# Optimization experiments

Measured on AMD Instinct MI355X. Metric: run time of the kernel, lower is better.

## Reference

```python
import jax, jax.numpy as jnp
import numpy as np

L = 8192      # residues
K = 48        # k_neighbors
NODE = 128    # node_features
EDGE = 128    # edge_features
RBF = 16      # rbf_dim
POS = 16      # pos_embed_dim
AA = 26       # amino-acid alphabet
EPS = 1e-6


def _rbf(D):
    # Gaussian radial basis lift on [2, 22] Angstrom, 16 bins (ProteinMPNN standard)
    mu = jnp.linspace(2.0, 22.0, RBF).astype(D.dtype)
    sigma = (22.0 - 2.0) / RBF
    return jnp.exp(-(((D[..., None] - mu) / sigma) ** 2))


def setup_inputs() -> dict:
    key = jax.random.key(0)
    ks = jax.random.split(key, 8)
    X = jax.random.normal(ks[0], (L, 3), dtype=jnp.float32) * 10.0
    node_h = jax.random.normal(ks[1], (L, NODE), dtype=jnp.float32)
    f_node = jax.random.normal(ks[2], (L, EDGE), dtype=jnp.float32)
    aatype = jax.random.randint(ks[3], (L,), 0, AA, dtype=jnp.int32)
    residue_index = jnp.arange(L, dtype=jnp.int32)
    Wpos = jax.random.normal(ks[4], (16, POS + RBF + 8 + AA), dtype=jnp.float32) * 0.05
    bpos = jnp.zeros((16,), jnp.float32)
    We = jax.random.normal(ks[5], (EDGE, EDGE + 16 + RBF + NODE + NODE), dtype=jnp.float32) * 0.05
    ln_scale = jnp.ones((EDGE,), jnp.float32)
    ln_bias = jnp.zeros((EDGE,), jnp.float32)
    Wproj = jax.random.normal(ks[6], (EDGE, EDGE), dtype=jnp.float32) * 0.05
    bproj = jnp.zeros((EDGE,), jnp.float32)
    return dict(X=X, node_h=node_h, f_node=f_node, Wpos=Wpos, bpos=bpos, We=We,
                ln_scale=ln_scale, ln_bias=ln_bias, Wproj=Wproj, bproj=bproj,
                aatype=aatype, residue_index=residue_index)


def reference(X, node_h, f_node, Wpos, bpos, We, ln_scale, ln_bias, Wproj, bproj,
              aatype, residue_index):
    # pairwise CA distances [L, L] and k nearest neighbors
    diff_all = X[:, None, :] - X[None, :, :]
    D = jnp.sqrt(jnp.sum(diff_all * diff_all, -1) + EPS)
    negk, idx = jax.lax.top_k(-D, K)          # idx: [L, K]
    Dk = -negk                                # [L, K] neighbor distances
    rbf = _rbf(Dk)                            # [L, K, 16]
    # clipped relative sequence position one-hot [L, K, 16]
    off = residue_index[idx] - residue_index[:, None]
    pos_emb = jax.nn.one_hot(jnp.clip(off + POS // 2, 0, POS - 1), POS, dtype=X.dtype)
    # 8 geometric scalars: 5 distance transforms + unit direction vector
    unit = (X[idx] - X[:, None, :]) / (Dk[..., None] + EPS)
    scal = jnp.stack([Dk / 10.0, 1.0 / (1.0 + Dk), jnp.exp(-Dk), jnp.sin(Dk), jnp.cos(Dk)], -1)
    geom = jnp.concatenate([scal, unit], -1)  # [L, K, 8]
    seq_j = jax.nn.one_hot(aatype[idx], AA, dtype=X.dtype)  # [L, K, 26]
    pos_in = jnp.concatenate([pos_emb, rbf, geom, seq_j], -1)  # [L, K, 66]
    e_pos = pos_in @ Wpos.T + bpos            # w_pos: [L, K, 16]
    h_i = jnp.broadcast_to(node_h[:, None, :], (L, K, NODE))
    e_in = jnp.concatenate([f_node[idx], e_pos, rbf, h_i, node_h[idx]], -1)  # [L, K, 416]
    e = e_in @ We.T                           # w_e (no bias): [L, K, EDGE]
    mean = jnp.mean(e, -1, keepdims=True)
    var = jnp.var(e, -1, keepdims=True)
    e = (e - mean) * jax.lax.rsqrt(var + 1e-5) * ln_scale + ln_bias  # norm_edges
    return e @ Wproj.T + bproj                # w_e_proj: [L, K, EDGE]
```

## Files before the change

### kernel.cpp

```cpp
#include <hip/hip_runtime.h>
#include <stdint.h>
#include <math.h>

#define LRES 8192
#define KNB  48
#define ASTR 296
#define CUT  64

typedef _Float16 half_t;
typedef _Float16 half8 __attribute__((ext_vector_type(8)));
typedef float f4 __attribute__((ext_vector_type(4)));

__global__ void prep_kernel(const float* __restrict__ We, const float* __restrict__ Wproj,
                            const float* __restrict__ Wpos,
                            half_t* __restrict__ WeH, half_t* __restrict__ WpH,
                            float* __restrict__ Wh32, half_t* __restrict__ WposB) {
  int t = blockIdx.x * blockDim.x + threadIdx.x;
  if (t < 128 * 288) {
    int n = t / 288, kp = t % 288;
    int k = kp < 160 ? kp : kp + 128;
    WeH[n * 288 + kp] = (half_t)We[n * 416 + k];
  }
  if (t < 128 * 128) {
    int n = t >> 7, k = t & 127;
    WpH[t] = (half_t)Wproj[t];
    Wh32[k * 128 + n] = We[n * 416 + 160 + k];
  }
  if (t < 512) {
    int p = t >> 5, k = t & 31;
    float v = (k < 8) ? Wpos[p * 66 + 32 + k] : ((k < 16) ? 0.0f : Wpos[p * 66 + k]);
    WposB[t] = (half_t)v;
  }
}

__global__ __launch_bounds__(256) void cvt_kernel(const float* __restrict__ f_node,
                                                  const float* __restrict__ node_h,
                                                  half_t* __restrict__ fnH,
                                                  half_t* __restrict__ nhH) {
  int g = blockIdx.x * 256 + threadIdx.x;
  int sel = g >> 17;
  size_t off = (size_t)(g & 131071) * 8;
  const float* s = sel ? node_h : f_node;
  half_t* d = sel ? nhH : fnH;
  f4 a = *(const f4*)(s + off);
  f4 b = *(const f4*)(s + off + 4);
  half8 h;
#pragma unroll
  for (int j = 0; j < 4; ++j) { h[j] = (half_t)a[j]; h[4 + j] = (half_t)b[j]; }
  *(half8*)(d + off) = h;
}

__global__ __launch_bounds__(256) void hbias_kernel(const float* __restrict__ node_h,
                                                    const float* __restrict__ Wh32,
                                                    float* __restrict__ hb) {
  __shared__ float hrow[4][128];
  const int i0 = blockIdx.x * 4;
  const int t = threadIdx.x;
  for (int u = t; u < 512; u += 256) hrow[u >> 7][u & 127] = node_h[(size_t)i0 * 128 + u];
  __syncthreads();
  const int n = t & 127, g = t >> 7;
  float s0 = 0.f, s1 = 0.f;
#pragma unroll 8
  for (int cc = 0; cc < 128; ++cc) {
    float w = Wh32[cc * 128 + n];
    s0 = fmaf(w, hrow[g][cc], s0);
    s1 = fmaf(w, hrow[g + 2][cc], s1);
  }
  hb[(size_t)(i0 + g) * 128 + n] = s0;
  hb[(size_t)(i0 + g + 2) * 128 + n] = s1;
}

__global__ __launch_bounds__(256) void knn_kernel(const float* __restrict__ X,
                                                  int* __restrict__ out_idx,
                                                  float* __restrict__ out_D) {
  __shared__ unsigned hist[256];
  __shared__ double candD[256];
  __shared__ int candJ[256];
  __shared__ unsigned cnt;
  __shared__ int bstar_s;
  __shared__ unsigned cexp_s;
  __shared__ int needFull_s;
  const int i = blockIdx.x;
  const int tid = threadIdx.x;
  const float xi = X[i * 3 + 0], yi = X[i * 3 + 1], zi = X[i * 3 + 2];
  hist[tid] = 0u;
  if (tid == 0) cnt = 0u;
  __syncthreads();
  unsigned bpack[8];
#pragma unroll
  for (int it = 0; it < 8; ++it) {
    int jb = (tid + it * 256) * 4;
    const float* xp = X + (size_t)jb * 3;
    f4 r0 = *(const f4*)(xp);
    f4 r1 = *(const f4*)(xp + 4);
    f4 r2 = *(const f4*)(xp + 8);
    float px[4] = {r0[0], r0[3], r1[2], r2[1]};
    float py[4] = {r0[1], r1[0], r1[3], r2[2]};
    float pz[4] = {r0[2], r1[1], r2[0], r2[3]};
#pragma unroll
    for (int q = 0; q < 4; ++q) {
      float dx = px[q] - xi, dy = py[q] - yi, dz = pz[q] - zi;
      float D = sqrtf(dx * dx + dy * dy + dz * dz + 1e-6f);
      int b = (int)(D * 4.0f); if (b > 255) b = 255;
      int idx = it * 4 + q;
      int sh = (idx & 3) * 8;
      if ((idx & 3) == 0) bpack[idx >> 2] = (unsigned)b; else bpack[idx >> 2] |= (unsigned)b << sh;
      if (b < CUT) atomicAdd(&hist[b], 1u);
    }
  }
  __syncthreads();
  if (tid == 0) {
    unsigned run = 0; int b = 0;
    while (b < 255 && run + hist[b] < KNB) { run += hist[b]; ++b; }
    bstar_s = b;
    needFull_s = (b >= CUT - 1) ? 1 : 0;
    unsigned tot = run + hist[b];
    if (b < 255) tot += hist[b + 1];
    cexp_s = tot;
  }
  __syncthreads();
  if (needFull_s) {
#pragma unroll
    for (int idx = 0; idx < 32; ++idx) {
      int b = (int)((bpack[idx >> 2] >> ((idx & 3) * 8)) & 0xFFu);
      if (b >= CUT) atomicAdd(&hist[b], 1u);
    }
    __syncthreads();
    if (tid == 0) {
      unsigned run = 0; int b = 0;
      while (b < 255 && run + hist[b] < KNB) { run += hist[b]; ++b; }
      bstar_s = b;
      unsigned tot = run + hist[b];
      if (b < 255) tot += hist[b + 1];
      cexp_s = tot;
    }
    __syncthreads();
  }
  int bthr = bstar_s + 1; if (bthr > 255) bthr = 255;
  const unsigned cexp = cexp_s;
  const double xid = (double)xi, yid = (double)yi, zid = (double)zi;
  {
    unsigned cmask = 0u;
#pragma unroll
    for (int idx = 0; idx < 32; ++idx) {
      int b = (int)((bpack[idx >> 2] >> ((idx & 3) * 8)) & 0xFFu);
      if (b <= bthr) cmask |= (1u << idx);
    }
    while (cmask) {
      int k = __builtin_ctz(cmask);
      cmask &= cmask - 1u;
      int j = (tid + (k >> 2) * 256) * 4 + (k & 3);
      unsigned p = atomicAdd(&cnt, 1u);
      if (p < 256u) {
        double ddx = (double)X[j * 3 + 0] - xid;
        double ddy = (double)X[j * 3 + 1] - yid;
        double ddz = (double)X[j * 3 + 2] - zid;
        candD[p] = sqrt(ddx * ddx + ddy * ddy + ddz * ddz + 1e-6);
        candJ[p] = j;
      }
    }
  }
  __syncthreads();
  unsigned n = cnt;
  if (cexp <= 64u) {
    if (tid < 64) {
      double d = (tid < (int)n) ? candD[tid] : INFINITY;
      int j = (tid < (int)n) ? candJ[tid] : 0x7FFFFFFF;
#pragma unroll
      for (int size = 2; size <= 64; size <<= 1) {
#pragma unroll
        for (int stride = 32; stride > 0; stride >>= 1) {
          if (stride >= size) continue;
          double dp = __shfl_xor(d, stride, 64);
          int jp = __shfl_xor(j, stride, 64);
          bool up = ((tid & size) == 0);
          bool lower = ((tid & stride) == 0);
          bool mine_gt = (d > dp) || (d == dp && j > jp);
          bool part_gt = (dp > d) || (dp == d && jp > j);
          bool keep = lower ? (mine_gt != up) : (part_gt != up);
          d = keep ? d : dp;
          j = keep ? j : jp;
        }
      }
      if (tid < KNB) {
        out_idx[(size_t)i * KNB + tid] = j;
        out_D[(size_t)i * KNB + tid] = (float)d;
      }
    }
    return;
  }
  if (tid >= (int)n) { candD[tid] = INFINITY; candJ[tid] = 0x7FFFFFFF; }
  __syncthreads();
  for (unsigned size = 2; size <= 256; size <<= 1) {
    for (unsigned stride = size >> 1; stride > 0; stride >>= 1) {
      unsigned partner = (unsigned)tid ^ stride;
      if (partner > (unsigned)tid) {
        double da = candD[tid], db = candD[partner];
        int ja = candJ[tid], jb = candJ[partner];
        bool agtb = (da > db) || (da == db && ja > jb);
        bool asc = ((tid & size) == 0);
        if (agtb == asc) {
          candD[tid] = db; candJ[tid] = jb;
          candD[partner] = da; candJ[partner] = ja;
        }
      }
      __syncthreads();
    }
  }
  if (tid < KNB) {
    out_idx[(size_t)i * KNB + tid] = candJ[tid];
    out_D[(size_t)i * KNB + tid] = (float)candD[tid];
  }
}

__global__ __launch_bounds__(256, 4) void edge_kernel(
    const float* __restrict__ X, const half_t* __restrict__ fnH,
    const half_t* __restrict__ nhH, const float* __restrict__ Wpos,
    const float* __restrict__ bpos, const float* __restrict__ ln_scale,
    const float* __restrict__ ln_bias, const float* __restrict__ bproj,
    const int* __restrict__ aatype, const int* __restrict__ residue_index,
    const int* __restrict__ ws_idx, const float* __restrict__ ws_D,
    const half_t* __restrict__ WeH, const half_t* __restrict__ WpH,
    const half_t* __restrict__ WposB, const float* __restrict__ hbAll,
    float* __restrict__ out) {
  __shared__ __align__(16) half_t Ald[48 * ASTR];
  __shared__ float tabPool[672];
  __shared__ float DkL[48];
  __shared__ int jL[48], pidxL[48], aaL[48];

  float* pos_tab = tabPool;
  float* aa_tab  = tabPool + 256;
  float* redS    = tabPool;
  float* meanL   = tabPool + 384;
  float* rstdL   = tabPool + 432;

  const int i = blockIdx.x;
  const int tid = threadIdx.x;
  const int w = tid >> 6;
  const int lane = tid & 63;
  const int lm = lane & 15;
  const int quad = lane >> 4;
  const int quad8 = quad * 8;
  const int n0 = w * 32 + lm;

  {
    int pp = tid >> 4, p = tid & 15;
    pos_tab[tid] = Wpos[p * 66 + pp] + bpos[p];
  }
  for (int t = tid; t < 416; t += 256) {
    int a = t >> 4, p = t & 15;
    aa_tab[t] = Wpos[p * 66 + 40 + a];
  }
  const float xi = X[i * 3 + 0], yi = X[i * 3 + 1], zi = X[i * 3 + 2];
  if (tid < KNB) {
    int e = tid;
    int j = ws_idx[(size_t)i * KNB + e];
    float Dk = ws_D[(size_t)i * KNB + e];
    jL[e] = j; DkL[e] = Dk;
    float xj = X[j * 3 + 0], yj = X[j * 3 + 1], zj = X[j * 3 + 2];
    float inv = 1.0f / (Dk + 1e-6f);
    half_t* gr = Ald + e * ASTR + 128;
    gr[0] = (half_t)(Dk / 10.0f);
    gr[1] = (half_t)(1.0f / (1.0f + Dk));
    gr[2] = (half_t)expf(-Dk);
    gr[3] = (half_t)sinf(Dk);
    gr[4] = (half_t)cosf(Dk);
    gr[5] = (half_t)((xj - xi) * inv);
    gr[6] = (half_t)((yj - yi) * inv);
    gr[7] = (half_t)((zj - zi) * inv);
    *(uint2*)(gr + 8)  = (uint2){0u, 0u};
    *(uint2*)(gr + 12) = (uint2){0u, 0u};
    int off = residue_index[j] - residue_index[i] + 8;
    off = off < 0 ? 0 : (off > 15 ? 15 : off);
    pidxL[e] = off;
    aaL[e] = aatype[j];
  }
  __syncthreads();

  for (int t = tid; t < KNB * 16; t += 256) {
    int e = t >> 4, m = t & 15;
    float z = (DkL[e] - (2.0f + (float)m * (20.0f / 15.0f))) * 0.8f;
    Ald[e * ASTR + 144 + m] = (half_t)expf(-z * z);
  }
#pragma unroll
  for (int it = 0; it < 6; ++it) {
    int cid = tid + it * 256;
    int e = cid >> 5, r = cid & 31;
    int sel = r >> 4, c8 = r & 15;
    const half_t* src = (sel ? nhH : fnH) + (size_t)jL[e] * 128 + c8 * 8;
    *(half8*)(Ald + e * ASTR + sel * 160 + c8 * 8) = *(const half8*)src;
  }
  half8 bregA[9], bregB[9];
#pragma unroll
  for (int ks = 0; ks < 9; ++ks) {
    bregA[ks] = *(const half8*)(WeH + (size_t)n0 * 288 + ks * 32 + quad8);
    bregB[ks] = *(const half8*)(WeH + (size_t)(n0 + 16) * 288 + ks * 32 + quad8);
  }
  float hb0 = hbAll[(size_t)i * 128 + n0];
  float hb1 = hbAll[(size_t)i * 128 + n0 + 16];
  __syncthreads();

  if (w < 3) {
    half8 a = *(const half8*)(Ald + (w * 16 + lm) * ASTR + 128 + quad8);
    half8 bp = *(const half8*)(WposB + lm * 32 + quad8);
    f4 z = {};
    f4 ep = __builtin_amdgcn_mfma_f32_16x16x32_f16(a, bp, z, 0, 0, 0);
#pragma unroll
    for (int r = 0; r < 4; ++r) {
      int m = w * 16 + quad * 4 + r;
      float s = ep[r] + pos_tab[pidxL[m] * 16 + lm] + aa_tab[aaL[m] * 16 + lm];
      Ald[m * ASTR + 128 + lm] = (half_t)s;
    }
  }
  __syncthreads();

  f4 acc[3][2] = {};
#pragma unroll
  for (int ks = 0; ks < 9; ++ks) {
#pragma unroll
    for (int mt = 0; mt < 3; ++mt) {
      half8 a = *(const half8*)(Ald + (mt * 16 + lm) * ASTR + ks * 32 + quad8);
      acc[mt][0] = __builtin_amdgcn_mfma_f32_16x16x32_f16(a, bregA[ks], acc[mt][0], 0, 0, 0);
      acc[mt][1] = __builtin_amdgcn_mfma_f32_16x16x32_f16(a, bregB[ks], acc[mt][1], 0, 0, 0);
    }
  }
  half8 b2A[4], b2B[4];
#pragma unroll
  for (int ks = 0; ks < 4; ++ks) {
    b2A[ks] = *(const half8*)(WpH + (size_t)n0 * 128 + ks * 32 + quad8);
    b2B[ks] = *(const half8*)(WpH + (size_t)(n0 + 16) * 128 + ks * 32 + quad8);
  }
  float ls0 = ln_scale[n0], ls1 = ln_scale[n0 + 16];
  float lb0 = ln_bias[n0],  lb1 = ln_bias[n0 + 16];
  float bp0 = bproj[n0],    bp1 = bproj[n0 + 16];

#pragma unroll
  for (int mt = 0; mt < 3; ++mt)
#pragma unroll
    for (int r = 0; r < 4; ++r) { acc[mt][0][r] += hb0; acc[mt][1][r] += hb1; }
#pragma unroll
  for (int mt = 0; mt < 3; ++mt)
#pragma unroll
    for (int r = 0; r < 4; ++r) {
      float e0 = acc[mt][0][r], e1 = acc[mt][1][r];
      float sv = e0 + e1;
      float qv = e0 * e0 + e1 * e1;
#pragma unroll
      for (int m = 1; m < 16; m <<= 1) {
        sv += __shfl_xor(sv, m, 16);
        qv += __shfl_xor(qv, m, 16);
      }
      if (lm == 0) {
        int row = mt * 16 + quad * 4 + r;
        redS[row * 8 + w * 2 + 0] = sv;
        redS[row * 8 + w * 2 + 1] = qv;
      }
    }
  __syncthreads();
  if (tid < KNB) {
    float s = redS[tid * 8 + 0] + redS[tid * 8 + 2] + redS[tid * 8 + 4] + redS[tid * 8 + 6];
    float q = redS[tid * 8 + 1] + redS[tid * 8 + 3] + redS[tid * 8 + 5] + redS[tid * 8 + 7];
    float m = s * (1.0f / 128.0f);
    float var = q * (1.0f / 128.0f) - m * m;
    meanL[tid] = m;
    rstdL[tid] = rsqrtf(var + 1e-5f);
  }
  __syncthreads();

#pragma unroll
  for (int mt = 0; mt < 3; ++mt)
#pragma unroll
    for (int nt = 0; nt < 2; ++nt) {
      int n = n0 + nt * 16;
      float ls = nt ? ls1 : ls0, lb = nt ? lb1 : lb0;
#pragma unroll
      for (int r = 0; r < 4; ++r) {
        int m = mt * 16 + quad * 4 + r;
        float e = (acc[mt][nt][r] - meanL[m]) * rstdL[m] * ls + lb;
        Ald[m * ASTR + n] = (half_t)e;
      }
    }
  __syncthreads();

  f4 acc2[3][2] = {};
#pragma unroll
  for (int ks = 0; ks < 4; ++ks) {
#pragma unroll
    for (int mt = 0; mt < 3; ++mt) {
      half8 a = *(const half8*)(Ald + (mt * 16 + lm) * ASTR + ks * 32 + quad8);
      acc2[mt][0] = __builtin_amdgcn_mfma_f32_16x16x32_f16(a, b2A[ks], acc2[mt][0], 0, 0, 0);
      acc2[mt][1] = __builtin_amdgcn_mfma_f32_16x16x32_f16(a, b2B[ks], acc2[mt][1], 0, 0, 0);
    }
  }

#pragma unroll
  for (int mt = 0; mt < 3; ++mt)
#pragma unroll
    for (int nt = 0; nt < 2; ++nt) {
      int n = n0 + nt * 16;
      float bp = nt ? bp1 : bp0;
#pragma unroll
      for (int r = 0; r < 4; ++r) {
        int m = mt * 16 + quad * 4 + r;
        out[((size_t)i * KNB + m) * 128 + n] = acc2[mt][nt][r] + bp;
      }
    }
}

extern "C" void kernel_launch(void* const* d_in, const int* in_sizes, int n_in,
                              void* d_out, int out_size, void* d_ws, size_t ws_size,
                              hipStream_t stream) {
  const float* X        = (const float*)d_in[0];
  const float* node_h   = (const float*)d_in[1];
  const float* f_node   = (const float*)d_in[2];
  const float* Wpos     = (const float*)d_in[3];
  const float* bpos     = (const float*)d_in[4];
  const float* We       = (const float*)d_in[5];
  const float* ln_scale = (const float*)d_in[6];
  const float* ln_bias  = (const float*)d_in[7];
  const float* Wproj    = (const float*)d_in[8];
  const float* bproj    = (const float*)d_in[9];
  const int*   aatype   = (const int*)d_in[10];
  const int*   residue_index = (const int*)d_in[11];
  float* out = (float*)d_out;

  char* ws = (char*)d_ws;
  int*    ws_idx = (int*)ws;
  float*  ws_D   = (float*)(ws + 1572864);
  half_t* WeH    = (half_t*)(ws + 3145728);
  half_t* WpH    = (half_t*)(ws + 3219456);
  float*  Wh32   = (float*)(ws + 3252224);
  half_t* WposB  = (half_t*)(ws + 3317760);
  float*  hbAll  = (float*)(ws + 3318784);
  half_t* fnH    = (half_t*)(ws + 7513088);
  half_t* nhH    = (half_t*)(ws + 9610240);

  prep_kernel<<<144, 256, 0, stream>>>(We, Wproj, Wpos, WeH, WpH, Wh32, WposB);
  cvt_kernel<<<1024, 256, 0, stream>>>(f_node, node_h, fnH, nhH);
  hbias_kernel<<<2048, 256, 0, stream>>>(node_h, Wh32, hbAll);
  knn_kernel<<<LRES, 256, 0, stream>>>(X, ws_idx, ws_D);
  edge_kernel<<<LRES, 256, 0, stream>>>(X, fnH, nhH, Wpos, bpos, ln_scale,
                                        ln_bias, bproj, aatype, residue_index,
                                        ws_idx, ws_D, WeH, WpH, WposB, hbAll, out);
}
```

Measured before the change: 401.1 us.

## Fuse kNN selection into edge kernel and merge conversion with node-bias kernel

Merges the per-residue kNN kernel into the edge kernel so neighbor indices and distances stay in shared memory rather than passing through global workspace. The candidate sort buffers alias the edge input tile. The fp16 conversion and node-bias kernels are also combined into one launch. This removes two launches and a global round trip, but the fused kernel now carries kNN's work and register pressure under the edge kernel's occupancy bound, so the two phases cannot overlap across kernels.

```diff
diff --git a/kernel.cpp b/kernel.cpp
--- a/kernel.cpp
+++ b/kernel.cpp
@@ -11,10 +11,11 @@
 typedef _Float16 half8 __attribute__((ext_vector_type(8)));
 typedef float f4 __attribute__((ext_vector_type(4)));
 
-__global__ void prep_kernel(const float* __restrict__ We, const float* __restrict__ Wproj,
-                            const float* __restrict__ Wpos,
-                            half_t* __restrict__ WeH, half_t* __restrict__ WpH,
-                            float* __restrict__ Wh32, half_t* __restrict__ WposB) {
+__global__ __launch_bounds__(256) void setup_a_kernel(
+    const float* __restrict__ We, const float* __restrict__ Wproj,
+    const float* __restrict__ Wpos,
+    half_t* __restrict__ WeH, half_t* __restrict__ WpH,
+    float* __restrict__ Wh32, half_t* __restrict__ WposB) {
   int t = blockIdx.x * blockDim.x + threadIdx.x;
   if (t < 128 * 288) {
     int n = t / 288, kp = t % 288;
@@ -33,55 +34,88 @@
   }
 }
 
-__global__ __launch_bounds__(256) void cvt_kernel(const float* __restrict__ f_node,
-                                                  const float* __restrict__ node_h,
-                                                  half_t* __restrict__ fnH,
-                                                  half_t* __restrict__ nhH) {
-  int g = blockIdx.x * 256 + threadIdx.x;
-  int sel = g >> 17;
-  size_t off = (size_t)(g & 131071) * 8;
-  const float* s = sel ? node_h : f_node;
-  half_t* d = sel ? nhH : fnH;
-  f4 a = *(const f4*)(s + off);
-  f4 b = *(const f4*)(s + off + 4);
-  half8 h;
-#pragma unroll
-  for (int j = 0; j < 4; ++j) { h[j] = (half_t)a[j]; h[4 + j] = (half_t)b[j]; }
-  *(half8*)(d + off) = h;
+__global__ __launch_bounds__(256) void setup_b_kernel(
+    const float* __restrict__ f_node, const float* __restrict__ node_h,
+    const float* __restrict__ Wh32,
+    half_t* __restrict__ fnH, half_t* __restrict__ nhH,
+    float* __restrict__ hb) {
+  __shared__ float hrow[4][128];
+  const int b = blockIdx.x;
+  const int tid = threadIdx.x;
+  if (b < 1024) {
+    int g = b * 256 + tid;
+    int sel = g >> 17;
+    size_t off = (size_t)(g & 131071) * 8;
+    const float* s = sel ? node_h : f_node;
+    half_t* d = sel ? nhH : fnH;
+    f4 a = *(const f4*)(s + off);
+    f4 bb = *(const f4*)(s + off + 4);
+    half8 h;
+#pragma unroll
+    for (int j = 0; j < 4; ++j) { h[j] = (half_t)a[j]; h[4 + j] = (half_t)bb[j]; }
+    *(half8*)(d + off) = h;
+  } else {
+    const int i0 = (b - 1024) * 4;
+    for (int u = tid; u < 512; u += 256) hrow[u >> 7][u & 127] = node_h[(size_t)i0 * 128 + u];
+    __syncthreads();
+    const int n = tid & 127, g = tid >> 7;
+    float s0 = 0.f, s1 = 0.f;
+#pragma unroll 8
+    for (int cc = 0; cc < 128; ++cc) {
+      float w = Wh32[cc * 128 + n];
+      s0 = fmaf(w, hrow[g][cc], s0);
+      s1 = fmaf(w, hrow[g + 2][cc], s1);
+    }
+    hb[(size_t)(i0 + g) * 128 + n] = s0;
+    hb[(size_t)(i0 + g + 2) * 128 + n] = s1;
+  }
 }
 
-__global__ __launch_bounds__(256) void hbias_kernel(const float* __restrict__ node_h,
-                                                    const float* __restrict__ Wh32,
-                                                    float* __restrict__ hb) {
-  __shared__ float hrow[4][128];
-  const int i0 = blockIdx.x * 4;
-  const int t = threadIdx.x;
-  for (int u = t; u < 512; u += 256) hrow[u >> 7][u & 127] = node_h[(size_t)i0 * 128 + u];
-  __syncthreads();
-  const int n = t & 127, g = t >> 7;
-  float s0 = 0.f, s1 = 0.f;
-#pragma unroll 8
-  for (int cc = 0; cc < 128; ++cc) {
-    float w = Wh32[cc * 128 + n];
-    s0 = fmaf(w, hrow[g][cc], s0);
-    s1 = fmaf(w, hrow[g + 2][cc], s1);
-  }
-  hb[(size_t)(i0 + g) * 128 + n] = s0;
-  hb[(size_t)(i0 + g + 2) * 128 + n] = s1;
-}
-
-__global__ __launch_bounds__(256) void knn_kernel(const float* __restrict__ X,
-                                                  int* __restrict__ out_idx,
-                                                  float* __restrict__ out_D) {
+__global__ __launch_bounds__(256, 4) void fused_kernel(
+    const float* __restrict__ X, const half_t* __restrict__ fnH,
+    const half_t* __restrict__ nhH, const float* __restrict__ Wpos,
+    const float* __restrict__ bpos, const float* __restrict__ ln_scale,
+    const float* __restrict__ ln_bias, const float* __restrict__ bproj,
+    const int* __restrict__ aatype, const int* __restrict__ residue_index,
+    const half_t* __restrict__ WeH, const half_t* __restrict__ WpH,
+    const half_t* __restrict__ WposB, const float* __restrict__ hbAll,
+    float* __restrict__ out) {
+  __shared__ __align__(16) half_t Ald[48 * ASTR];
+  __shared__ float tabPool[672];
+  __shared__ float DkL[48];
+  __shared__ int jL[48], pidxL[48], aaL[48];
   __shared__ unsigned hist[256];
-  __shared__ double candD[256];
-  __shared__ int candJ[256];
   __shared__ unsigned cnt;
   __shared__ int bstar_s;
   __shared__ unsigned cexp_s;
   __shared__ int needFull_s;
+
+  double* candD = (double*)Ald;
+  int*    candJ = (int*)(Ald + 1024);
+  float* pos_tab = tabPool;
+  float* aa_tab  = tabPool + 256;
+  float* redS    = tabPool;
+  float* meanL   = tabPool + 384;
+  float* rstdL   = tabPool + 432;
+
   const int i = blockIdx.x;
   const int tid = threadIdx.x;
+  const int w = tid >> 6;
+  const int lane = tid & 63;
+  const int lm = lane & 15;
+  const int quad = lane >> 4;
+  const int quad8 = quad * 8;
+  const int n0 = w * 32 + lm;
+
+  {
+    int pp = tid >> 4, p = tid & 15;
+    pos_tab[tid] = Wpos[p * 66 + pp] + bpos[p];
+  }
+  for (int t = tid; t < 416; t += 256) {
+    int a = t >> 4, p = t & 15;
+    aa_tab[t] = Wpos[p * 66 + 40 + a];
+  }
+
   const float xi = X[i * 3 + 0], yi = X[i * 3 + 1], zi = X[i * 3 + 2];
   hist[tid] = 0u;
   if (tid == 0) cnt = 0u;
@@ -161,11 +195,11 @@
     }
   }
   __syncthreads();
-  unsigned n = cnt;
+  unsigned nc = cnt;
   if (cexp <= 64u) {
     if (tid < 64) {
-      double d = (tid < (int)n) ? candD[tid] : INFINITY;
-      int j = (tid < (int)n) ? candJ[tid] : 0x7FFFFFFF;
+      double d = (tid < (int)nc) ? candD[tid] : INFINITY;
+      int j = (tid < (int)nc) ? candJ[tid] : 0x7FFFFFFF;
 #pragma unroll
       for (int size = 2; size <= 64; size <<= 1) {
 #pragma unroll
@@ -182,81 +216,35 @@
           j = keep ? j : jp;
         }
       }
-      if (tid < KNB) {
-        out_idx[(size_t)i * KNB + tid] = j;
-        out_D[(size_t)i * KNB + tid] = (float)d;
-      }
-    }
-    return;
-  }
-  if (tid >= (int)n) { candD[tid] = INFINITY; candJ[tid] = 0x7FFFFFFF; }
-  __syncthreads();
-  for (unsigned size = 2; size <= 256; size <<= 1) {
-    for (unsigned stride = size >> 1; stride > 0; stride >>= 1) {
-      unsigned partner = (unsigned)tid ^ stride;
-      if (partner > (unsigned)tid) {
-        double da = candD[tid], db = candD[partner];
-        int ja = candJ[tid], jb = candJ[partner];
-        bool agtb = (da > db) || (da == db && ja > jb);
-        bool asc = ((tid & size) == 0);
-        if (agtb == asc) {
-          candD[tid] = db; candJ[tid] = jb;
-          candD[partner] = da; candJ[partner] = ja;
+      if (tid < KNB) { jL[tid] = j; DkL[tid] = (float)d; }
+    }
+  } else {
+    if (tid >= (int)nc) { candD[tid] = INFINITY; candJ[tid] = 0x7FFFFFFF; }
+    __syncthreads();
+    for (unsigned size = 2; size <= 256; size <<= 1) {
+      for (unsigned stride = size >> 1; stride > 0; stride >>= 1) {
+        unsigned partner = (unsigned)tid ^ stride;
+        if (partner > (unsigned)tid) {
+          double da = candD[tid], db = candD[partner];
+          int ja = candJ[tid], jb = candJ[partner];
+          bool agtb = (da > db) || (da == db && ja > jb);
+          bool asc = ((tid & size) == 0);
+          if (agtb == asc) {
+            candD[tid] = db; candJ[tid] = jb;
+            candD[partner] = da; candJ[partner] = ja;
+          }
         }
-      }
-      __syncthreads();
-    }
-  }
-  if (tid < KNB) {
-    out_idx[(size_t)i * KNB + tid] = candJ[tid];
-    out_D[(size_t)i * KNB + tid] = (float)candD[tid];
-  }
-}
-
-__global__ __launch_bounds__(256, 4) void edge_kernel(
-    const float* __restrict__ X, const half_t* __restrict__ fnH,
-    const half_t* __restrict__ nhH, const float* __restrict__ Wpos,
-    const float* __restrict__ bpos, const float* __restrict__ ln_scale,
-    const float* __restrict__ ln_bias, const float* __restrict__ bproj,
-    const int* __restrict__ aatype, const int* __restrict__ residue_index,
-    const int* __restrict__ ws_idx, const float* __restrict__ ws_D,
-    const half_t* __restrict__ WeH, const half_t* __restrict__ WpH,
-    const half_t* __restrict__ WposB, const float* __restrict__ hbAll,
-    float* __restrict__ out) {
-  __shared__ __align__(16) half_t Ald[48 * ASTR];
-  __shared__ float tabPool[672];
-  __shared__ float DkL[48];
-  __shared__ int jL[48], pidxL[48], aaL[48];
-
-  float* pos_tab = tabPool;
-  float* aa_tab  = tabPool + 256;
-  float* redS    = tabPool;
-  float* meanL   = tabPool + 384;
-  float* rstdL   = tabPool + 432;
-
-  const int i = blockIdx.x;
-  const int tid = threadIdx.x;
-  const int w = tid >> 6;
-  const int lane = tid & 63;
-  const int lm = lane & 15;
-  const int quad = lane >> 4;
-  const int quad8 = quad * 8;
-  const int n0 = w * 32 + lm;
-
-  {
-    int pp = tid >> 4, p = tid & 15;
-    pos_tab[tid] = Wpos[p * 66 + pp] + bpos[p];
-  }
-  for (int t = tid; t < 416; t += 256) {
-    int a = t >> 4, p = t & 15;
-    aa_tab[t] = Wpos[p * 66 + 40 + a];
-  }
-  const float xi = X[i * 3 + 0], yi = X[i * 3 + 1], zi = X[i * 3 + 2];
+        __syncthreads();
+      }
+    }
+    if (tid < KNB) { jL[tid] = candJ[tid]; DkL[tid] = (float)candD[tid]; }
+  }
+  __syncthreads();
+
   if (tid < KNB) {
     int e = tid;
-    int j = ws_idx[(size_t)i * KNB + e];
-    float Dk = ws_D[(size_t)i * KNB + e];
-    jL[e] = j; DkL[e] = Dk;
+    int j = jL[e];
+    float Dk = DkL[e];
     float xj = X[j * 3 + 0], yj = X[j * 3 + 1], zj = X[j * 3 + 2];
     float inv = 1.0f / (Dk + 1e-6f);
     half_t* gr = Ald + e * ASTR + 128;
@@ -425,8 +413,6 @@
   float* out = (float*)d_out;
 
   char* ws = (char*)d_ws;
-  int*    ws_idx = (int*)ws;
-  float*  ws_D   = (float*)(ws + 1572864);
   half_t* WeH    = (half_t*)(ws + 3145728);
   half_t* WpH    = (half_t*)(ws + 3219456);
   float*  Wh32   = (float*)(ws + 3252224);
@@ -435,11 +421,9 @@
   half_t* fnH    = (half_t*)(ws + 7513088);
   half_t* nhH    = (half_t*)(ws + 9610240);
 
-  prep_kernel<<<144, 256, 0, stream>>>(We, Wproj, Wpos, WeH, WpH, Wh32, WposB);
-  cvt_kernel<<<1024, 256, 0, stream>>>(f_node, node_h, fnH, nhH);
-  hbias_kernel<<<2048, 256, 0, stream>>>(node_h, Wh32, hbAll);
-  knn_kernel<<<LRES, 256, 0, stream>>>(X, ws_idx, ws_D);
-  edge_kernel<<<LRES, 256, 0, stream>>>(X, fnH, nhH, Wpos, bpos, ln_scale,
-                                        ln_bias, bproj, aatype, residue_index,
-                                        ws_idx, ws_D, WeH, WpH, WposB, hbAll, out);
+  setup_a_kernel<<<144, 256, 0, stream>>>(We, Wproj, Wpos, WeH, WpH, Wh32, WposB);
+  setup_b_kernel<<<3072, 256, 0, stream>>>(f_node, node_h, Wh32, fnH, nhH, hbAll);
+  fused_kernel<<<LRES, 256, 0, stream>>>(X, fnH, nhH, Wpos, bpos, ln_scale,
+                                         ln_bias, bproj, aatype, residue_index,
+                                         WeH, WpH, WposB, hbAll, out);
 }
```

After: 402.4 us. Within noise of the previous version (+0.3%).
